# Kernel optimization log

Measured on AMD Instinct MI355X. Metric: run time of the kernel, lower is better.

Reference implementation:

```python
import jax, jax.numpy as jnp
import numpy as np

B, T, C, H = 2, 2048, 2048, 16
HD = C // H      # 128 head dim
P = C // 8       # 256 octonion component width
NEG_INF = jnp.finfo(jnp.float32).min

# Cayley octonion multiplication table: e_i * e_j = OCT_SIGN[i,j] * e_{OCT_IDX[i,j]}
OCT_SIGN = np.array([
    [1, 1, 1, 1, 1, 1, 1, 1],
    [1,-1, 1,-1, 1,-1,-1, 1],
    [1,-1,-1, 1, 1, 1,-1,-1],
    [1, 1,-1,-1, 1,-1, 1,-1],
    [1,-1,-1,-1,-1, 1, 1, 1],
    [1, 1,-1, 1,-1,-1,-1, 1],
    [1, 1, 1,-1,-1, 1,-1,-1],
    [1,-1, 1, 1,-1,-1, 1,-1]], dtype=np.float32)
OCT_IDX = np.array([
    [0,1,2,3,4,5,6,7],
    [1,0,3,2,5,4,7,6],
    [2,3,0,1,6,7,4,5],
    [3,2,1,0,7,6,5,4],
    [4,5,6,7,0,1,2,3],
    [5,4,7,6,1,0,3,2],
    [6,7,4,5,2,3,0,1],
    [7,6,5,4,3,2,1,0]], dtype=np.int32)
_comb = np.zeros((8, 8, 8), np.float32)
for _i in range(8):
    for _j in range(8):
        _comb[OCT_IDX[_i, _j], _i, _j] = OCT_SIGN[_i, _j]
COMB = jnp.asarray(_comb)  # (k, i, j): out_k += sign * (W_i @ x_j)


def ternary(W):
    # BitNet-style ternary quantization with straight-through estimator
    s = jnp.mean(jnp.abs(W)) + 1e-8
    q = jnp.round(jnp.clip(W / s, -1.0, 1.0)) * s
    return W + jax.lax.stop_gradient(q - W)


def oct_linear(x, W):
    # x: (B,T,C), W: (8,P,P) -> (B,T,C)
    parts = jnp.stack(jnp.split(x, 8, axis=-1), axis=0)  # (8,B,T,P)
    Wq = ternary(W)
    prod = jnp.einsum('jbtp,ipq->ijbtq', parts, Wq)       # (8,8,B,T,P)
    out = jnp.einsum('kij,ijbtq->kbtq', COMB, prod)       # (8,B,T,P)
    return jnp.transpose(out, (1, 2, 0, 3)).reshape(x.shape[0], x.shape[1], C)


def rope(x, cos, sin):
    # x: (B,T,H,HD); cos/sin: (T, HD//2). Interleaved complex pairs as in view_as_complex.
    xr = x[..., 0::2]
    xi = x[..., 1::2]
    c = cos[None, :x.shape[1], None, :]
    s = sin[None, :x.shape[1], None, :]
    out = jnp.stack([xr * c - xi * s, xr * s + xi * c], axis=-1)
    return out.reshape(x.shape)


def setup_inputs() -> dict:
    key = jax.random.key(0)
    ks = jax.random.split(key, 5)
    x = jax.random.normal(ks[0], (B, T, C), dtype=jnp.float32)
    wq = jax.random.normal(ks[1], (8, P, P), dtype=jnp.float32) * 0.02
    wk = jax.random.normal(ks[2], (8, P, P), dtype=jnp.float32) * 0.02
    wv = jax.random.normal(ks[3], (8, P, P), dtype=jnp.float32) * 0.02
    wo = jax.random.normal(ks[4], (8, P, P), dtype=jnp.float32) * 0.02
    inv = 1.0 / (10000.0 ** (np.arange(0, HD, 2, dtype=np.float32) / HD))
    ang = np.outer(np.arange(T, dtype=np.float32), inv)
    freqs_cos = jnp.asarray(np.cos(ang), dtype=jnp.float32)
    freqs_sin = jnp.asarray(np.sin(ang), dtype=jnp.float32)
    return {"x": x, "wq": wq, "wk": wk, "wv": wv, "wo": wo,
            "freqs_cos": freqs_cos, "freqs_sin": freqs_sin}


def reference(x, wq, wk, wv, wo, freqs_cos, freqs_sin):
    b, t, _ = x.shape
    q = oct_linear(x, wq).reshape(b, t, H, HD)
    k = oct_linear(x, wk).reshape(b, t, H, HD)
    v = oct_linear(x, wv).reshape(b, t, H, HD)
    q = rope(q, freqs_cos, freqs_sin)
    k = rope(k, freqs_cos, freqs_sin)
    q = jnp.transpose(q, (0, 2, 1, 3))  # (B,H,T,HD)
    k = jnp.transpose(k, (0, 2, 1, 3))
    v = jnp.transpose(v, (0, 2, 1, 3))
    scores = jnp.einsum('bhtd,bhsd->bhts', q, k) / jnp.sqrt(jnp.float32(HD))
    mask = jnp.tril(jnp.ones((t, t), dtype=bool))
    scores = jnp.where(mask[None, None], scores, NEG_INF)
    attn = jax.nn.softmax(scores, axis=-1)
    y = jnp.einsum('bhts,bhsd->bhtd', attn, v)
    y = jnp.transpose(y, (0, 2, 1, 3)).reshape(b, t, C)
    return oct_linear(y, wo)
```

## Files before the change

kernel.cpp:

```cpp
#include <hip/hip_runtime.h>


typedef __attribute__((ext_vector_type(8))) short short8;
typedef __attribute__((ext_vector_type(4))) float f32x4;
typedef unsigned short u16;
typedef unsigned int u32;

__device__ __forceinline__ float bf2f(u16 u) {
    u32 x = ((u32)u) << 16;
    return __builtin_bit_cast(float, x);
}
__device__ __forceinline__ u16 f2bf(float f) {
    u32 x = __builtin_bit_cast(u32, f);
    x += 0x7fffu + ((x >> 16) & 1u);
    return (u16)(x >> 16);
}
__device__ __forceinline__ u16 f2bf_trunc(float f) {
    return (u16)(__builtin_bit_cast(u32, f) >> 16);
}
__device__ __forceinline__ u32 pack2(u16 a, u16 b) { return (u32)a | ((u32)b << 16); }

__device__ __forceinline__ void async16(const void* g, void* l) {
    __builtin_amdgcn_global_load_lds((const __attribute__((address_space(1))) u32*)g,
                                     (__attribute__((address_space(3))) u32*)l, 16, 0, 0);
}

__device__ const int d_OCT_IDX[8][8] = {
    {0,1,2,3,4,5,6,7},{1,0,3,2,5,4,7,6},{2,3,0,1,6,7,4,5},{3,2,1,0,7,6,5,4},
    {4,5,6,7,0,1,2,3},{5,4,7,6,1,0,3,2},{6,7,4,5,2,3,0,1},{7,6,5,4,3,2,1,0}};
__device__ const float d_OCT_SIGN[8][8] = {
    { 1, 1, 1, 1, 1, 1, 1, 1},{ 1,-1, 1,-1, 1,-1,-1, 1},{ 1,-1,-1, 1, 1, 1,-1,-1},
    { 1, 1,-1,-1, 1,-1, 1,-1},{ 1,-1,-1,-1,-1, 1, 1, 1},{ 1, 1,-1, 1,-1,-1,-1, 1},
    { 1, 1, 1,-1,-1, 1,-1,-1},{ 1,-1, 1, 1,-1,-1, 1,-1}};

__global__ __launch_bounds__(256) void reduce1_kernel(
    const float* __restrict__ w0, const float* __restrict__ w1,
    const float* __restrict__ w2, const float* __restrict__ w3,
    float* __restrict__ partials) {
    int bid = blockIdx.x, wsel = bid >> 6, part = bid & 63;
    const float* W = wsel == 0 ? w0 : wsel == 1 ? w1 : wsel == 2 ? w2 : w3;
    int base = part * 8192 + threadIdx.x;
    float acc = 0.f;
#pragma unroll
    for (int k = 0; k < 32; k++) acc += fabsf(W[base + k * 256]);
#pragma unroll
    for (int off = 1; off < 64; off <<= 1) acc += __shfl_xor(acc, off, 64);
    __shared__ float r4[4];
    if ((threadIdx.x & 63) == 0) r4[threadIdx.x >> 6] = acc;
    __syncthreads();
    if (threadIdx.x == 0) partials[bid] = r4[0] + r4[1] + r4[2] + r4[3];
}
__global__ __launch_bounds__(256) void reduce2_kernel(const float* __restrict__ partials,
                                                      float* __restrict__ s_vals) {
    int w = threadIdx.x >> 6, lane = threadIdx.x & 63;
    float v = partials[w * 64 + lane];
#pragma unroll
    for (int off = 1; off < 64; off <<= 1) v += __shfl_xor(v, off, 64);
    if (lane == 0) s_vals[w] = v / 524288.0f + 1e-8f;
}

__global__ __launch_bounds__(256) void cast_bf16_kernel(const float* __restrict__ X, u16* __restrict__ Xb) {
    int gid = blockIdx.x * 256 + threadIdx.x;
    const float4* X4 = (const float4*)X;
    float4 a = X4[gid * 2], b = X4[gid * 2 + 1];
    uint4 o;
    o.x = pack2(f2bf(a.x), f2bf(a.y));
    o.y = pack2(f2bf(a.z), f2bf(a.w));
    o.z = pack2(f2bf(b.x), f2bf(b.y));
    o.w = pack2(f2bf(b.z), f2bf(b.w));
    *(uint4*)&Xb[gid * 8] = o;
}

__global__ __launch_bounds__(256) void build_weff_kernel(
    const float* __restrict__ W, const float* __restrict__ sptr, u16* __restrict__ WT) {
    __shared__ float Tt[64 * 68];
    int tid = threadIdx.x;
    int combo = blockIdx.x >> 4, sub = blockIdx.x & 15;
    int j = combo >> 3, kblk = combo & 7;
    int i = 0;
#pragma unroll
    for (int ii = 0; ii < 8; ii++)
        if (d_OCT_IDX[ii][j] == kblk) i = ii;
    float sign = d_OCT_SIGN[i][j];
    int p0 = (sub >> 2) * 64, q0 = (sub & 3) * 64;
    float inv_s = 1.0f / (*sptr);
#pragma unroll
    for (int pass = 0; pass < 4; pass++) {
        int p = p0 + pass * 16 + (tid >> 4);
        int q = q0 + (tid & 15) * 4;
        float4 wv = *(const float4*)&W[i * 65536 + p * 256 + q];
        float* Tp = &Tt[(pass * 16 + (tid >> 4)) * 68 + (tid & 15) * 4];
        Tp[0] = sign * rintf(fminf(1.f, fmaxf(-1.f, wv.x * inv_s)));
        Tp[1] = sign * rintf(fminf(1.f, fmaxf(-1.f, wv.y * inv_s)));
        Tp[2] = sign * rintf(fminf(1.f, fmaxf(-1.f, wv.z * inv_s)));
        Tp[3] = sign * rintf(fminf(1.f, fmaxf(-1.f, wv.w * inv_s)));
    }
    __syncthreads();
#pragma unroll
    for (int pass = 0; pass < 2; pass++) {
        int qq = pass * 32 + (tid >> 3);
        int pl = (tid & 7) * 8;
        u16 r[8];
#pragma unroll
        for (int l = 0; l < 8; l++) r[l] = f2bf_trunc(Tt[(pl + l) * 68 + qq]);
        uint4 o;
        o.x = pack2(r[0], r[1]); o.y = pack2(r[2], r[3]);
        o.z = pack2(r[4], r[5]); o.w = pack2(r[6], r[7]);
        *(uint4*)&WT[(size_t)(kblk * 256 + q0 + qq) * 2048 + j * 256 + p0 + pl] = o;
    }
}

template <int MODE>
__global__ __launch_bounds__(256) void gemm_kernel(
    const u16* __restrict__ A, const u16* __restrict__ Bt,
    const float* __restrict__ sptr, void* __restrict__ Cout) {
    __shared__ __align__(16) u16 As[2][128 * 64];
    __shared__ __align__(16) u16 Bs[2][128 * 64];
    const int K = 2048;
    const int NIT = K / 64;
    int tid = threadIdx.x, lane = tid & 63, wid = tid >> 6;
    int quad = lane >> 4, l16 = lane & 15;
    int wm = (wid >> 1) * 64, wn = (wid & 1) * 64;
    int m0 = blockIdx.y * 128, n0 = blockIdx.x * 128;
    f32x4 acc[4][4];
#pragma unroll
    for (int a = 0; a < 4; a++)
#pragma unroll
        for (int b = 0; b < 4; b++) acc[a][b] = (f32x4){0.f, 0.f, 0.f, 0.f};
    int sr = lane >> 3, sb = lane & 7;
    const u16* Ag = A + (size_t)(m0 + wid * 32 + sr) * K + ((sb ^ sr) * 8);
    const u16* Bg = Bt + (size_t)(n0 + wid * 32 + sr) * K + ((sb ^ sr) * 8);
#pragma unroll
    for (int cc = 0; cc < 4; cc++) {
        async16(Ag + (size_t)cc * 8 * K, &As[0][(wid * 32 + cc * 8) * 64]);
        async16(Bg + (size_t)cc * 8 * K, &Bs[0][(wid * 32 + cc * 8) * 64]);
    }
    for (int g = 0; g < NIT; g++) {
        int c = g & 1;
        __syncthreads();
        if (g + 1 < NIT) {
            int k1 = (g + 1) * 64;
#pragma unroll
            for (int cc = 0; cc < 4; cc++) {
                async16(Ag + k1 + (size_t)cc * 8 * K, &As[1 - c][(wid * 32 + cc * 8) * 64]);
                async16(Bg + k1 + (size_t)cc * 8 * K, &Bs[1 - c][(wid * 32 + cc * 8) * 64]);
            }
        }
#pragma unroll
        for (int kc = 0; kc < 2; kc++) {
            short8 af[4], bfv[4];
#pragma unroll
            for (int mt = 0; mt < 4; mt++)
                af[mt] = *(const short8*)&As[c][(wm + mt * 16 + l16) * 64 + (((kc << 2) | quad) ^ (l16 & 7)) * 8];
#pragma unroll
            for (int nt = 0; nt < 4; nt++)
                bfv[nt] = *(const short8*)&Bs[c][(wn + nt * 16 + l16) * 64 + (((kc << 2) | quad) ^ (l16 & 7)) * 8];
#pragma unroll
            for (int mt = 0; mt < 4; mt++)
#pragma unroll
                for (int nt = 0; nt < 4; nt++)
                    acc[mt][nt] = __builtin_amdgcn_mfma_f32_16x16x32_bf16(af[mt], bfv[nt], acc[mt][nt], 0, 0, 0);
        }
    }
    float s = *sptr;
#pragma unroll
    for (int mt = 0; mt < 4; mt++)
#pragma unroll
        for (int nt = 0; nt < 4; nt++) {
            int mg = m0 + wm + mt * 16 + quad * 4;
            int ng = n0 + wn + nt * 16 + l16;
            if (MODE == 0) {
#pragma unroll
                for (int r = 0; r < 4; r++)
                    ((u16*)Cout)[(size_t)(mg + r) * 2048 + ng] = f2bf(acc[mt][nt][r] * s);
            } else if (MODE == 1) {
#pragma unroll
                for (int r = 0; r < 4; r++)
                    ((float*)Cout)[(size_t)(mg + r) * 2048 + ng] = acc[mt][nt][r] * s;
            } else {
                ushort4 o4;
                o4.x = f2bf(acc[mt][nt][0] * s);
                o4.y = f2bf(acc[mt][nt][1] * s);
                o4.z = f2bf(acc[mt][nt][2] * s);
                o4.w = f2bf(acc[mt][nt][3] * s);
                *(ushort4*)&((u16*)Cout)[((size_t)((mg >> 11) * 16 + (ng >> 7)) * 128 + (ng & 127)) * 2048 + (mg & 2047)] = o4;
            }
        }
}

__device__ __forceinline__ u32 rope_rot(u32 u, float c, float s) {
    float xr = bf2f((u16)(u & 0xffff));
    float xi = bf2f((u16)(u >> 16));
    return pack2(f2bf(xr * c - xi * s), f2bf(xr * s + xi * c));
}
__global__ __launch_bounds__(256) void rope_kernel(
    u16* __restrict__ Xb, const float* __restrict__ fc, const float* __restrict__ fs, float scale) {
    int gid = blockIdx.x * 256 + threadIdx.x;
    int e0 = gid * 4;
    int t = (e0 >> 10) & 2047;
    int m = e0 & 63;
    uint4 u = ((const uint4*)Xb)[gid];
    float4 c4 = *(const float4*)&fc[t * 64 + m];
    float4 s4 = *(const float4*)&fs[t * 64 + m];
    uint4 o;
    o.x = rope_rot(u.x, c4.x * scale, s4.x * scale);
    o.y = rope_rot(u.y, c4.y * scale, s4.y * scale);
    o.z = rope_rot(u.z, c4.z * scale, s4.z * scale);
    o.w = rope_rot(u.w, c4.w * scale, s4.w * scale);
    ((uint4*)Xb)[gid] = o;
}

__global__ __launch_bounds__(512, 4) void flash_kernel(
    const u16* __restrict__ Q, const u16* __restrict__ Kg,
    const u16* __restrict__ VTg, u16* __restrict__ Y) {
    __shared__ __align__(16) u16 Ks[2][64 * 128];
    __shared__ __align__(16) u16 Vs[128 * 64];
    __shared__ __align__(16) u16 Ps[8 * 16 * 64];
    const int NIT = 34;
    int tid = threadIdx.x, lane = tid & 63, wid = tid >> 6;
    int quad = lane >> 4, l16 = lane & 15;
    int bh = blockIdx.x, b = bh >> 4, h = bh & 15;
    int qt = blockIdx.y;
    int nitA = 2 * qt + 2;
    const u16* Qb = Q + (size_t)b * 2048 * 2048 + h * 128;
    const u16* Kb = Kg + (size_t)b * 2048 * 2048 + h * 128;
    const u16* Vb = VTg + (size_t)bh * 128 * 2048;
    int q0 = qt * 128, nit = nitA;
    int ksr = lane >> 4, ksb = lane & 15;
    int vd0 = wid * 16 + (lane >> 3), vkb = lane & 7;
#pragma unroll
    for (int cc = 0; cc < 2; cc++) {
        int ch = wid * 2 + cc;
        int kr = ch * 4 + ksr;
        async16(&Kb[(size_t)kr * 2048 + (ksb ^ (kr & 15)) * 8], &Ks[0][ch * 512]);
    }
    uint4 vreg[2];
    vreg[0] = *(const uint4*)&Vb[(size_t)vd0 * 2048 + vkb * 8];
    vreg[1] = *(const uint4*)&Vb[(size_t)(vd0 + 8) * 2048 + vkb * 8];
    short8 qf[4];
#pragma unroll
    for (int kt = 0; kt < 4; kt++)
        qf[kt] = *(const short8*)&Qb[(size_t)(q0 + wid * 16 + l16) * 2048 + kt * 32 + quad * 8];
    f32x4 o[8];
#pragma unroll
    for (int nt = 0; nt < 8; nt++) o[nt] = (f32x4){0.f, 0.f, 0.f, 0.f};
    float m_[4] = {-1e30f, -1e30f, -1e30f, -1e30f};
    float l_[4] = {0.f, 0.f, 0.f, 0.f};
    int il = 0;
    for (int g = 0; g < NIT; g++) {
        int c = g & 1;
        __syncthreads();
        *(uint4*)&Vs[vd0 * 64 + (vkb ^ (vd0 & 7)) * 8] = vreg[0];
        *(uint4*)&Vs[(vd0 + 8) * 64 + (vkb ^ ((vd0 + 8) & 7)) * 8] = vreg[1];
        if (g + 1 < NIT) {
            int gn = g + 1;
            int s0n = (gn < nitA ? gn : gn - nitA) * 64;
#pragma unroll
            for (int cc = 0; cc < 2; cc++) {
                int ch = wid * 2 + cc;
                int kr = ch * 4 + ksr;
                async16(&Kb[(size_t)(s0n + kr) * 2048 + (ksb ^ (kr & 15)) * 8], &Ks[1 - c][ch * 512]);
            }
            vreg[0] = *(const uint4*)&Vb[(size_t)vd0 * 2048 + s0n + vkb * 8];
            vreg[1] = *(const uint4*)&Vb[(size_t)(vd0 + 8) * 2048 + s0n + vkb * 8];
        }
        int s0 = il * 64;
        f32x4 sc[4];
#pragma unroll
        for (int ct = 0; ct < 4; ct++) {
            f32x4 a = (f32x4){0.f, 0.f, 0.f, 0.f};
#pragma unroll
            for (int kt = 0; kt < 4; kt++) {
                short8 bfv = *(const short8*)&Ks[c][(ct * 16 + l16) * 128 + ((kt * 4 + quad) ^ l16) * 8];
                a = __builtin_amdgcn_mfma_f32_16x16x32_bf16(qf[kt], bfv, a, 0, 0, 0);
            }
            sc[ct] = a;
        }
        if (il >= nit - 2) {
#pragma unroll
            for (int ct = 0; ct < 4; ct++) {
                int colg = s0 + ct * 16 + l16;
#pragma unroll
                for (int r = 0; r < 4; r++) {
                    int rowg = q0 + wid * 16 + quad * 4 + r;
                    if (colg > rowg) sc[ct][r] = -1e30f;
                }
            }
        }
        float mx[4];
#pragma unroll
        for (int r = 0; r < 4; r++) {
            float m2 = fmaxf(fmaxf(sc[0][r], sc[1][r]), fmaxf(sc[2][r], sc[3][r]));
#pragma unroll
            for (int off = 1; off < 16; off <<= 1) m2 = fmaxf(m2, __shfl_xor(m2, off, 64));
            mx[r] = m2;
        }
        bool need = (mx[0] > m_[0] + 8.f) || (mx[1] > m_[1] + 8.f) ||
                    (mx[2] > m_[2] + 8.f) || (mx[3] > m_[3] + 8.f);
        if (__any(need)) {
            float alpha[4];
#pragma unroll
            for (int r = 0; r < 4; r++) {
                float mn = fmaxf(m_[r], mx[r]);
                alpha[r] = exp2f(m_[r] - mn);
                m_[r] = mn;
                l_[r] *= alpha[r];
            }
#pragma unroll
            for (int nt = 0; nt < 8; nt++)
#pragma unroll
                for (int r = 0; r < 4; r++) o[nt][r] *= alpha[r];
        }
#pragma unroll
        for (int r = 0; r < 4; r++) {
            float rs = 0.f;
#pragma unroll
            for (int ct = 0; ct < 4; ct++) {
                float p = exp2f(sc[ct][r] - m_[r]);
                sc[ct][r] = p;
                rs += p;
            }
#pragma unroll
            for (int off = 1; off < 16; off <<= 1) rs += __shfl_xor(rs, off, 64);
            l_[r] += rs;
        }
        u16* Pw = &Ps[wid * 1024];
#pragma unroll
        for (int ct = 0; ct < 4; ct++)
#pragma unroll
            for (int r = 0; r < 4; r++) {
                int lr = quad * 4 + r;
                int key = ct * 16 + l16;
                Pw[lr * 64 + ((key >> 3) ^ (lr & 7)) * 8 + (key & 7)] = f2bf_trunc(sc[ct][r]);
            }
        asm volatile("s_waitcnt lgkmcnt(0)" ::: "memory");
        __builtin_amdgcn_sched_barrier(0);
        __builtin_amdgcn_s_barrier();
#pragma unroll
        for (int kt2 = 0; kt2 < 2; kt2++) {
            short8 pa = *(const short8*)&Pw[l16 * 64 + ((kt2 * 4 + quad) ^ (l16 & 7)) * 8];
#pragma unroll
            for (int nt = 0; nt < 8; nt++) {
                short8 vb = *(const short8*)&Vs[(nt * 16 + l16) * 64 + ((kt2 * 4 + quad) ^ (l16 & 7)) * 8];
                o[nt] = __builtin_amdgcn_mfma_f32_16x16x32_bf16(pa, vb, o[nt], 0, 0, 0);
            }
        }
        il++;
        if (il == nit && g + 1 < NIT) {
            float iv[4];
#pragma unroll
            for (int r = 0; r < 4; r++) iv[r] = 1.f / l_[r];
#pragma unroll
            for (int nt = 0; nt < 8; nt++)
#pragma unroll
                for (int r = 0; r < 4; r++) {
                    int t_ = q0 + wid * 16 + quad * 4 + r;
                    Y[((size_t)(b * 2048 + t_)) * 2048 + h * 128 + nt * 16 + l16] = f2bf(o[nt][r] * iv[r]);
                }
            q0 = (15 - qt) * 128;
            nit = NIT - nitA;
            il = 0;
#pragma unroll
            for (int kt = 0; kt < 4; kt++)
                qf[kt] = *(const short8*)&Qb[(size_t)(q0 + wid * 16 + l16) * 2048 + kt * 32 + quad * 8];
#pragma unroll
            for (int nt = 0; nt < 8; nt++) o[nt] = (f32x4){0.f, 0.f, 0.f, 0.f};
#pragma unroll
            for (int r = 0; r < 4; r++) { m_[r] = -1e30f; l_[r] = 0.f; }
        }
    }
    float iv[4];
#pragma unroll
    for (int r = 0; r < 4; r++) iv[r] = 1.f / l_[r];
#pragma unroll
    for (int nt = 0; nt < 8; nt++)
#pragma unroll
        for (int r = 0; r < 4; r++) {
            int t_ = q0 + wid * 16 + quad * 4 + r;
            Y[((size_t)(b * 2048 + t_)) * 2048 + h * 128 + nt * 16 + l16] = f2bf(o[nt][r] * iv[r]);
        }
}

extern "C" void kernel_launch(void* const* d_in, const int* in_sizes, int n_in,
                              void* d_out, int out_size, void* d_ws, size_t ws_size,
                              hipStream_t stream) {
    const float* x  = (const float*)d_in[0];
    const float* wq = (const float*)d_in[1];
    const float* wk = (const float*)d_in[2];
    const float* wv = (const float*)d_in[3];
    const float* wo = (const float*)d_in[4];
    const float* fc = (const float*)d_in[5];
    const float* fs = (const float*)d_in[6];
    float* out = (float*)d_out;

    char* ws = (char*)d_ws;
    float* s_vals   = (float*)ws;
    float* partials = (float*)(ws + 1024);
    u16* WT  = (u16*)(ws + 8192);
    u16* xb  = (u16*)(ws + 8192 + 8388608);
    u16* Qb  = xb + 8388608;
    u16* Kb  = Qb + 8388608;
    u16* VTb = Kb + 8388608;

    const float QSCALE = 0.08838834764831845f * 1.4426950408889634f;

    reduce1_kernel<<<256, 256, 0, stream>>>(wq, wk, wv, wo, partials);
    reduce2_kernel<<<1, 256, 0, stream>>>(partials, s_vals);
    cast_bf16_kernel<<<4096, 256, 0, stream>>>(x, xb);

    build_weff_kernel<<<1024, 256, 0, stream>>>(wq, s_vals + 0, WT);
    gemm_kernel<0><<<dim3(16, 32), 256, 0, stream>>>(xb, WT, s_vals + 0, Qb);
    rope_kernel<<<4096, 256, 0, stream>>>(Qb, fc, fs, QSCALE);

    build_weff_kernel<<<1024, 256, 0, stream>>>(wk, s_vals + 1, WT);
    gemm_kernel<0><<<dim3(16, 32), 256, 0, stream>>>(xb, WT, s_vals + 1, Kb);
    rope_kernel<<<4096, 256, 0, stream>>>(Kb, fc, fs, 1.0f);

    build_weff_kernel<<<1024, 256, 0, stream>>>(wv, s_vals + 2, WT);
    gemm_kernel<2><<<dim3(16, 32), 256, 0, stream>>>(xb, WT, s_vals + 2, VTb);

    flash_kernel<<<dim3(32, 8), 512, 0, stream>>>(Qb, Kb, VTb, Qb );

    build_weff_kernel<<<1024, 256, 0, stream>>>(wo, s_vals + 3, WT);
    gemm_kernel<1><<<dim3(16, 32), 256, 0, stream>>>(Qb, WT, s_vals + 3, (void*)out);
}
```

Baseline: 437.9 us.

## Batch weight builds and QKV GEMMs, fuse RoPE epilogue, async V loads

Combines the four ternary weight-build launches into one kernel. Merges the Q, K and V projections into a single 3D-grid GEMM whose epilogue applies RoPE and the Q scale through lane shuffles, which removes the separate rope passes over Q and K. In the flash kernel, V tiles now load asynchronously into double-buffered LDS, an explicit barrier is dropped, and launch bounds are relaxed to 2 blocks. The fused path needs a larger workspace and falls back to the old sequence otherwise. Dropping the barrier before the P·V reads from LDS could risk a race, although each wave reads only its own P slice.

```diff
diff --git a/kernel.cpp b/kernel.cpp
--- a/kernel.cpp
+++ b/kernel.cpp
@@ -71,11 +71,10 @@
     *(uint4*)&Xb[gid * 8] = o;
 }
 
-__global__ __launch_bounds__(256) void build_weff_kernel(
-    const float* __restrict__ W, const float* __restrict__ sptr, u16* __restrict__ WT) {
-    __shared__ float Tt[64 * 68];
-    int tid = threadIdx.x;
-    int combo = blockIdx.x >> 4, sub = blockIdx.x & 15;
+__device__ __forceinline__ void weff_body(const float* __restrict__ W, float inv_s,
+                                          u16* __restrict__ WT, int bid, int tid,
+                                          float* __restrict__ Tt) {
+    int combo = bid >> 4, sub = bid & 15;
     int j = combo >> 3, kblk = combo & 7;
     int i = 0;
 #pragma unroll
@@ -83,7 +82,6 @@
         if (d_OCT_IDX[ii][j] == kblk) i = ii;
     float sign = d_OCT_SIGN[i][j];
     int p0 = (sub >> 2) * 64, q0 = (sub & 3) * 64;
-    float inv_s = 1.0f / (*sptr);
 #pragma unroll
     for (int pass = 0; pass < 4; pass++) {
         int p = p0 + pass * 16 + (tid >> 4);
@@ -108,6 +106,23 @@
         o.z = pack2(r[4], r[5]); o.w = pack2(r[6], r[7]);
         *(uint4*)&WT[(size_t)(kblk * 256 + q0 + qq) * 2048 + j * 256 + p0 + pl] = o;
     }
+}
+
+__global__ __launch_bounds__(256) void build_weff_kernel(
+    const float* __restrict__ W, const float* __restrict__ sptr, u16* __restrict__ WT) {
+    __shared__ float Tt[64 * 68];
+    weff_body(W, 1.0f / (*sptr), WT, blockIdx.x, threadIdx.x, Tt);
+}
+
+__global__ __launch_bounds__(256) void build_all_kernel(
+    const float* __restrict__ w0, const float* __restrict__ w1,
+    const float* __restrict__ w2, const float* __restrict__ w3,
+    const float* __restrict__ s_vals, u16* __restrict__ WTbase) {
+    __shared__ float Tt[64 * 68];
+    int wsel = blockIdx.x >> 10;
+    const float* W = wsel == 0 ? w0 : wsel == 1 ? w1 : wsel == 2 ? w2 : w3;
+    weff_body(W, 1.0f / s_vals[wsel], WTbase + (size_t)wsel * 4194304,
+              blockIdx.x & 1023, threadIdx.x, Tt);
 }
 
 template <int MODE>
@@ -169,11 +184,7 @@
         for (int nt = 0; nt < 4; nt++) {
             int mg = m0 + wm + mt * 16 + quad * 4;
             int ng = n0 + wn + nt * 16 + l16;
-            if (MODE == 0) {
-#pragma unroll
-                for (int r = 0; r < 4; r++)
-                    ((u16*)Cout)[(size_t)(mg + r) * 2048 + ng] = f2bf(acc[mt][nt][r] * s);
-            } else if (MODE == 1) {
+            if (MODE == 1) {
 #pragma unroll
                 for (int r = 0; r < 4; r++)
                     ((float*)Cout)[(size_t)(mg + r) * 2048 + ng] = acc[mt][nt][r] * s;
@@ -188,33 +199,104 @@
         }
 }
 
-__device__ __forceinline__ u32 rope_rot(u32 u, float c, float s) {
-    float xr = bf2f((u16)(u & 0xffff));
-    float xi = bf2f((u16)(u >> 16));
-    return pack2(f2bf(xr * c - xi * s), f2bf(xr * s + xi * c));
-}
-__global__ __launch_bounds__(256) void rope_kernel(
-    u16* __restrict__ Xb, const float* __restrict__ fc, const float* __restrict__ fs, float scale) {
-    int gid = blockIdx.x * 256 + threadIdx.x;
-    int e0 = gid * 4;
-    int t = (e0 >> 10) & 2047;
-    int m = e0 & 63;
-    uint4 u = ((const uint4*)Xb)[gid];
-    float4 c4 = *(const float4*)&fc[t * 64 + m];
-    float4 s4 = *(const float4*)&fs[t * 64 + m];
-    uint4 o;
-    o.x = rope_rot(u.x, c4.x * scale, s4.x * scale);
-    o.y = rope_rot(u.y, c4.y * scale, s4.y * scale);
-    o.z = rope_rot(u.z, c4.z * scale, s4.z * scale);
-    o.w = rope_rot(u.w, c4.w * scale, s4.w * scale);
-    ((uint4*)Xb)[gid] = o;
-}
-
-__global__ __launch_bounds__(512, 4) void flash_kernel(
+__global__ __launch_bounds__(256) void gemm_qkv_kernel(
+    const u16* __restrict__ A, const u16* __restrict__ WT0,
+    const float* __restrict__ s_vals, u16* __restrict__ Cbase,
+    const float* __restrict__ fc, const float* __restrict__ fs, float qscale) {
+    __shared__ __align__(16) u16 As[2][128 * 64];
+    __shared__ __align__(16) u16 Bs[2][128 * 64];
+    const int K = 2048;
+    const int NIT = K / 64;
+    int z = blockIdx.z;
+    const u16* Bt = WT0 + (size_t)z * 4194304;
+    u16* Cout = Cbase + (size_t)z * 8388608;
+    int tid = threadIdx.x, lane = tid & 63, wid = tid >> 6;
+    int quad = lane >> 4, l16 = lane & 15;
+    int wm = (wid >> 1) * 64, wn = (wid & 1) * 64;
+    int m0 = blockIdx.y * 128, n0 = blockIdx.x * 128;
+    f32x4 acc[4][4];
+#pragma unroll
+    for (int a = 0; a < 4; a++)
+#pragma unroll
+        for (int b = 0; b < 4; b++) acc[a][b] = (f32x4){0.f, 0.f, 0.f, 0.f};
+    int sr = lane >> 3, sb = lane & 7;
+    const u16* Ag = A + (size_t)(m0 + wid * 32 + sr) * K + ((sb ^ sr) * 8);
+    const u16* Bg = Bt + (size_t)(n0 + wid * 32 + sr) * K + ((sb ^ sr) * 8);
+#pragma unroll
+    for (int cc = 0; cc < 4; cc++) {
+        async16(Ag + (size_t)cc * 8 * K, &As[0][(wid * 32 + cc * 8) * 64]);
+        async16(Bg + (size_t)cc * 8 * K, &Bs[0][(wid * 32 + cc * 8) * 64]);
+    }
+    for (int g = 0; g < NIT; g++) {
+        int c = g & 1;
+        __syncthreads();
+        if (g + 1 < NIT) {
+            int k1 = (g + 1) * 64;
+#pragma unroll
+            for (int cc = 0; cc < 4; cc++) {
+                async16(Ag + k1 + (size_t)cc * 8 * K, &As[1 - c][(wid * 32 + cc * 8) * 64]);
+                async16(Bg + k1 + (size_t)cc * 8 * K, &Bs[1 - c][(wid * 32 + cc * 8) * 64]);
+            }
+        }
+#pragma unroll
+        for (int kc = 0; kc < 2; kc++) {
+            short8 af[4], bfv[4];
+#pragma unroll
+            for (int mt = 0; mt < 4; mt++)
+                af[mt] = *(const short8*)&As[c][(wm + mt * 16 + l16) * 64 + (((kc << 2) | quad) ^ (l16 & 7)) * 8];
+#pragma unroll
+            for (int nt = 0; nt < 4; nt++)
+                bfv[nt] = *(const short8*)&Bs[c][(wn + nt * 16 + l16) * 64 + (((kc << 2) | quad) ^ (l16 & 7)) * 8];
+#pragma unroll
+            for (int mt = 0; mt < 4; mt++)
+#pragma unroll
+                for (int nt = 0; nt < 4; nt++)
+                    acc[mt][nt] = __builtin_amdgcn_mfma_f32_16x16x32_bf16(af[mt], bfv[nt], acc[mt][nt], 0, 0, 0);
+        }
+    }
+    float s = s_vals[z];
+    if (z < 2) {
+        float rsc = (z == 0) ? qscale : 1.0f;
+        float sgn = (l16 & 1) ? 1.f : -1.f;
+#pragma unroll
+        for (int mt = 0; mt < 4; mt++)
+#pragma unroll
+            for (int nt = 0; nt < 4; nt++) {
+                int mg = m0 + wm + mt * 16 + quad * 4;
+                int ng = n0 + wn + nt * 16 + l16;
+                int m = (ng >> 1) & 63;
+#pragma unroll
+                for (int r = 0; r < 4; r++) {
+                    float v = acc[mt][nt][r] * s;
+                    float pv = __shfl_xor(v, 1, 64);
+                    int t = (mg + r) & 2047;
+                    float cv = fc[t * 64 + m] * rsc;
+                    float sv = fs[t * 64 + m] * rsc;
+                    Cout[(size_t)(mg + r) * 2048 + ng] = f2bf(v * cv + pv * sv * sgn);
+                }
+            }
+    } else {
+#pragma unroll
+        for (int mt = 0; mt < 4; mt++)
+#pragma unroll
+            for (int nt = 0; nt < 4; nt++) {
+                int mg = m0 + wm + mt * 16 + quad * 4;
+                int ng = n0 + wn + nt * 16 + l16;
+                ushort4 o4;
+                o4.x = f2bf(acc[mt][nt][0] * s);
+                o4.y = f2bf(acc[mt][nt][1] * s);
+                o4.z = f2bf(acc[mt][nt][2] * s);
+                o4.w = f2bf(acc[mt][nt][3] * s);
+                *(ushort4*)&Cout[((size_t)((mg >> 11) * 16 + (ng >> 7)) * 128 + (ng & 127)) * 2048 + (mg & 2047)] = o4;
+            }
+    }
+}
+
+__global__ __launch_bounds__(512, 2) void flash_kernel(
     const u16* __restrict__ Q, const u16* __restrict__ Kg,
     const u16* __restrict__ VTg, u16* __restrict__ Y) {
     __shared__ __align__(16) u16 Ks[2][64 * 128];
-    __shared__ __align__(16) u16 Vs[128 * 64];
+    __shared__ __align__(16) u16 Vs[2][128 * 64];
     __shared__ __align__(16) u16 Ps[8 * 16 * 64];
     const int NIT = 34;
     int tid = threadIdx.x, lane = tid & 63, wid = tid >> 6;
@@ -227,16 +309,15 @@
     const u16* Vb = VTg + (size_t)bh * 128 * 2048;
     int q0 = qt * 128, nit = nitA;
     int ksr = lane >> 4, ksb = lane & 15;
-    int vd0 = wid * 16 + (lane >> 3), vkb = lane & 7;
+    int vsr = lane >> 3, vsb = lane & 7;
 #pragma unroll
     for (int cc = 0; cc < 2; cc++) {
         int ch = wid * 2 + cc;
         int kr = ch * 4 + ksr;
         async16(&Kb[(size_t)kr * 2048 + (ksb ^ (kr & 15)) * 8], &Ks[0][ch * 512]);
-    }
-    uint4 vreg[2];
-    vreg[0] = *(const uint4*)&Vb[(size_t)vd0 * 2048 + vkb * 8];
-    vreg[1] = *(const uint4*)&Vb[(size_t)(vd0 + 8) * 2048 + vkb * 8];
+        int vd = ch * 8 + vsr;
+        async16(&Vb[(size_t)vd * 2048 + (vsb ^ (vd & 7)) * 8], &Vs[0][ch * 512]);
+    }
     short8 qf[4];
 #pragma unroll
     for (int kt = 0; kt < 4; kt++)
@@ -250,8 +331,6 @@
     for (int g = 0; g < NIT; g++) {
         int c = g & 1;
         __syncthreads();
-        *(uint4*)&Vs[vd0 * 64 + (vkb ^ (vd0 & 7)) * 8] = vreg[0];
-        *(uint4*)&Vs[(vd0 + 8) * 64 + (vkb ^ ((vd0 + 8) & 7)) * 8] = vreg[1];
         if (g + 1 < NIT) {
             int gn = g + 1;
             int s0n = (gn < nitA ? gn : gn - nitA) * 64;
@@ -260,9 +339,9 @@
                 int ch = wid * 2 + cc;
                 int kr = ch * 4 + ksr;
                 async16(&Kb[(size_t)(s0n + kr) * 2048 + (ksb ^ (kr & 15)) * 8], &Ks[1 - c][ch * 512]);
-            }
-            vreg[0] = *(const uint4*)&Vb[(size_t)vd0 * 2048 + s0n + vkb * 8];
-            vreg[1] = *(const uint4*)&Vb[(size_t)(vd0 + 8) * 2048 + s0n + vkb * 8];
+                int vd = ch * 8 + vsr;
+                async16(&Vb[(size_t)vd * 2048 + s0n + (vsb ^ (vd & 7)) * 8], &Vs[1 - c][ch * 512]);
+            }
         }
         int s0 = il * 64;
         f32x4 sc[4];
@@ -298,18 +377,15 @@
         bool need = (mx[0] > m_[0] + 8.f) || (mx[1] > m_[1] + 8.f) ||
                     (mx[2] > m_[2] + 8.f) || (mx[3] > m_[3] + 8.f);
         if (__any(need)) {
-            float alpha[4];
 #pragma unroll
             for (int r = 0; r < 4; r++) {
                 float mn = fmaxf(m_[r], mx[r]);
-                alpha[r] = exp2f(m_[r] - mn);
+                float al = exp2f(m_[r] - mn);
                 m_[r] = mn;
-                l_[r] *= alpha[r];
-            }
-#pragma unroll
-            for (int nt = 0; nt < 8; nt++)
-#pragma unroll
-                for (int r = 0; r < 4; r++) o[nt][r] *= alpha[r];
+                l_[r] *= al;
+#pragma unroll
+                for (int nt = 0; nt < 8; nt++) o[nt][r] *= al;
+            }
         }
 #pragma unroll
         for (int r = 0; r < 4; r++) {
@@ -333,15 +409,12 @@
                 int key = ct * 16 + l16;
                 Pw[lr * 64 + ((key >> 3) ^ (lr & 7)) * 8 + (key & 7)] = f2bf_trunc(sc[ct][r]);
             }
-        asm volatile("s_waitcnt lgkmcnt(0)" ::: "memory");
-        __builtin_amdgcn_sched_barrier(0);
-        __builtin_amdgcn_s_barrier();
 #pragma unroll
         for (int kt2 = 0; kt2 < 2; kt2++) {
             short8 pa = *(const short8*)&Pw[l16 * 64 + ((kt2 * 4 + quad) ^ (l16 & 7)) * 8];
 #pragma unroll
             for (int nt = 0; nt < 8; nt++) {
-                short8 vb = *(const short8*)&Vs[(nt * 16 + l16) * 64 + ((kt2 * 4 + quad) ^ (l16 & 7)) * 8];
+                short8 vb = *(const short8*)&Vs[c][(nt * 16 + l16) * 64 + ((kt2 * 4 + quad) ^ (l16 & 7)) * 8];
                 o[nt] = __builtin_amdgcn_mfma_f32_16x16x32_bf16(pa, vb, o[nt], 0, 0, 0);
             }
         }
@@ -393,34 +466,51 @@
     const float* fs = (const float*)d_in[6];
     float* out = (float*)d_out;
 
+    const float QSCALE = 0.08838834764831845f * 1.4426950408889634f;
     char* ws = (char*)d_ws;
     float* s_vals   = (float*)ws;
     float* partials = (float*)(ws + 1024);
-    u16* WT  = (u16*)(ws + 8192);
-    u16* xb  = (u16*)(ws + 8192 + 8388608);
-    u16* Qb  = xb + 8388608;
-    u16* Kb  = Qb + 8388608;
-    u16* VTb = Kb + 8388608;
-
-    const float QSCALE = 0.08838834764831845f * 1.4426950408889634f;
-
-    reduce1_kernel<<<256, 256, 0, stream>>>(wq, wk, wv, wo, partials);
-    reduce2_kernel<<<1, 256, 0, stream>>>(partials, s_vals);
-    cast_bf16_kernel<<<4096, 256, 0, stream>>>(x, xb);
-
-    build_weff_kernel<<<1024, 256, 0, stream>>>(wq, s_vals + 0, WT);
-    gemm_kernel<0><<<dim3(16, 32), 256, 0, stream>>>(xb, WT, s_vals + 0, Qb);
-    rope_kernel<<<4096, 256, 0, stream>>>(Qb, fc, fs, QSCALE);
-
-    build_weff_kernel<<<1024, 256, 0, stream>>>(wk, s_vals + 1, WT);
-    gemm_kernel<0><<<dim3(16, 32), 256, 0, stream>>>(xb, WT, s_vals + 1, Kb);
-    rope_kernel<<<4096, 256, 0, stream>>>(Kb, fc, fs, 1.0f);
-
-    build_weff_kernel<<<1024, 256, 0, stream>>>(wv, s_vals + 2, WT);
-    gemm_kernel<2><<<dim3(16, 32), 256, 0, stream>>>(xb, WT, s_vals + 2, VTb);
-
-    flash_kernel<<<dim3(32, 8), 512, 0, stream>>>(Qb, Kb, VTb, Qb );
-
-    build_weff_kernel<<<1024, 256, 0, stream>>>(wo, s_vals + 3, WT);
-    gemm_kernel<1><<<dim3(16, 32), 256, 0, stream>>>(Qb, WT, s_vals + 3, (void*)out);
-}
+
+    const size_t FUSED_NEED = 8192 + 4ull * 8388608  + 16777216
+                            + 3ull * 16777216 ;
+    if (ws_size >= FUSED_NEED) {
+        u16* WT  = (u16*)(ws + 8192);
+        u16* xb  = WT + 4ull * 4194304;
+        u16* Qb  = xb + 8388608;
+        u16* Kb  = Qb + 8388608;
+        u16* VTb = Kb + 8388608;
+
+        reduce1_kernel<<<256, 256, 0, stream>>>(wq, wk, wv, wo, partials);
+        reduce2_kernel<<<1, 256, 0, stream>>>(partials, s_vals);
+        cast_bf16_kernel<<<4096, 256, 0, stream>>>(x, xb);
+        build_all_kernel<<<4096, 256, 0, stream>>>(wq, wk, wv, wo, s_vals, WT);
+        gemm_qkv_kernel<<<dim3(16, 32, 3), 256, 0, stream>>>(xb, WT, s_vals, Qb, fc, fs, QSCALE);
+        flash_kernel<<<dim3(32, 8), 512, 0, stream>>>(Qb, Kb, VTb, Qb );
+        gemm_kernel<1><<<dim3(16, 32), 256, 0, stream>>>(Qb, WT + 3ull * 4194304,
+                                                         s_vals + 3, (void*)out);
+    } else {
+        u16* WT  = (u16*)(ws + 8192);
+        u16* xb  = (u16*)(ws + 8192 + 8388608);
+        u16* Qb  = xb + 8388608;
+        u16* Kb  = Qb + 8388608;
+        u16* VTb = Kb + 8388608;
+
+        reduce1_kernel<<<256, 256, 0, stream>>>(wq, wk, wv, wo, partials);
+        reduce2_kernel<<<1, 256, 0, stream>>>(partials, s_vals);
+        cast_bf16_kernel<<<4096, 256, 0, stream>>>(x, xb);
+
+        build_weff_kernel<<<1024, 256, 0, stream>>>(wq, s_vals + 0, WT);
+        gemm_qkv_kernel<<<dim3(16, 32, 1), 256, 0, stream>>>(xb, WT, s_vals + 0, Qb, fc, fs, QSCALE);
+
+        build_weff_kernel<<<1024, 256, 0, stream>>>(wk, s_vals + 1, WT);
+        gemm_qkv_kernel<<<dim3(16, 32, 1), 256, 0, stream>>>(xb, WT, s_vals + 1, Kb, fc, fs, 1.0f);
+
+        build_weff_kernel<<<1024, 256, 0, stream>>>(wv, s_vals + 2, WT);
+        gemm_kernel<2><<<dim3(16, 32), 256, 0, stream>>>(xb, WT, s_vals + 2, VTb);
+
+        flash_kernel<<<dim3(32, 8), 512, 0, stream>>>(Qb, Kb, VTb, Qb);
+
+        build_weff_kernel<<<1024, 256, 0, stream>>>(wo, s_vals + 3, WT);
+        gemm_kernel<1><<<dim3(16, 32), 256, 0, stream>>>(Qb, WT, s_vals + 3, (void*)out);
+    }
+}
```

After: 363.7 us. 1.2x faster.
